# Kernel optimization log

Hardware: AMD Instinct MI355X
Metric: run time of the kernel (lower is better)

The kernel has to match this reference:

```python
import jax, jax.numpy as jnp
import numpy as np

B, C, H, W, S = 32, 512, 32, 32, 4
HW = H * W
OUT = HW // S  # conv1/conv2 out channels = 256
EPS = 1e-5


def setup_inputs() -> dict:
    key = jax.random.key(0)
    ks = jax.random.split(key, 8)
    d = {}
    d["x"] = jax.random.normal(ks[0], (B, C, H, W), jnp.float32)
    # conv1 / bn1 (operate on x_flat with 'channels' = h*w)
    d["w1"] = jax.random.normal(ks[1], (OUT, HW), jnp.float32) * 0.02
    d["b1"] = jnp.zeros((OUT,), jnp.float32)
    d["g1"] = jnp.ones((OUT,), jnp.float32)
    d["be1"] = jnp.zeros((OUT,), jnp.float32)
    d["m1"] = jax.random.normal(ks[2], (OUT,), jnp.float32) * 0.01
    d["v1"] = jnp.ones((OUT,), jnp.float32)
    # conv2 / bn2
    d["w2"] = jax.random.normal(ks[3], (OUT, HW), jnp.float32) * 0.02
    d["b2"] = jnp.zeros((OUT,), jnp.float32)
    d["g2"] = jnp.ones((OUT,), jnp.float32)
    d["be2"] = jnp.zeros((OUT,), jnp.float32)
    d["m2"] = jax.random.normal(ks[4], (OUT,), jnp.float32) * 0.01
    d["v2"] = jnp.ones((OUT,), jnp.float32)
    # conv3 / bn3 (1x1 conv on the real channel dim c)
    d["w3"] = jax.random.normal(ks[5], (C, C), jnp.float32) * 0.02
    d["b3"] = jnp.zeros((C,), jnp.float32)
    d["g3"] = jnp.ones((C,), jnp.float32)
    d["be3"] = jnp.zeros((C,), jnp.float32)
    d["m3"] = jax.random.normal(ks[6], (C,), jnp.float32) * 0.01
    d["v3"] = jnp.ones((C,), jnp.float32)
    # conv4: 1x1 conv mapping 1+2c channels -> 1
    d["w4"] = jax.random.normal(ks[7], (1 + 2 * C,), jnp.float32) * 0.02
    d["b4"] = jnp.zeros((), jnp.float32)
    return d


def _bn1d(t, g, be, m, v):
    # t: [b, o, c]; BatchNorm (eval mode) over channel axis 1
    scale = g / jnp.sqrt(v + EPS)
    return (t - m[:, None]) * scale[:, None] + be[:, None]


def reference(x, w1, b1, g1, be1, m1, v1,
              w2, b2, g2, be2, m2, v2,
              w3, b3, g3, be3, m3, v3,
              w4, b4):
    b, c, h, w = x.shape
    # x_flat: [b, h*w, c] -- conv1/conv2 are 1x1 convs over 'channels' = h*w
    xf = x.reshape(b, c, h * w).transpose(0, 2, 1)
    theta = jax.nn.relu(_bn1d(jnp.einsum('oq,bqc->boc', w1, xf) + b1[:, None],
                              g1, be1, m1, v1))  # [b, OUT, c]
    phi = jax.nn.relu(_bn1d(jnp.einsum('oq,bqc->boc', w2, xf) + b2[:, None],
                            g2, be2, m2, v2))    # [b, OUT, c]
    # per-batch conv2d-as-matmul loop collapses to one batched GEMM:
    # affinity[b, i, j] = sum_k phi[b, k, i] * theta[b, k, j]
    aff = jnp.einsum('bki,bkj->bij', phi, theta)  # [b, c, c]
    # x_embed: 1x1 conv + BN + ReLU + global average pool -> [b, c]
    scale3 = g3 / jnp.sqrt(v3 + EPS)
    xe = jnp.einsum('oc,bchw->bohw', w3, x) + b3[:, None, None]
    xe = jax.nn.relu((xe - m3[:, None, None]) * scale3[:, None, None]
                     + be3[:, None, None])
    xe = xe.mean(axis=(2, 3))  # [b, c]
    # conv4 over y = cat([x_embed, affinity_a, affinity_b], dim=1):
    # affinity_a[b,i,0,p] = aff[b,i,p]; affinity_b[b,i,0,p] = aff[b,p,i]
    logits = (w4[0] * xe
              + jnp.einsum('i,bip->bp', w4[1:1 + c], aff)
              + jnp.einsum('i,bpi->bp', w4[1 + c:], aff)
              + b4)
    a = jax.nn.sigmoid(logits)  # [b, c]
    return x * a[:, :, None, None]
```

## Files before the change

kernel.cpp:

```cpp
#include <hip/hip_runtime.h>
#include <math.h>

#define BB   32
#define CC   512
#define HWW  1024
#define OUTC 256
#define EPSV 1e-5f

typedef __attribute__((ext_vector_type(8))) short bfrag;
typedef __attribute__((ext_vector_type(4))) float f32x4;

__device__ inline unsigned short f2bf(float x){
  unsigned int uu = __float_as_uint(x);
  uu += 0x7fff + ((uu >> 16) & 1);
  return (unsigned short)(uu >> 16);
}
__device__ inline float bf2f(unsigned short h){
  return __uint_as_float(((unsigned int)h) << 16);
}

#define ASYNC16(g, l) \
  __builtin_amdgcn_global_load_lds((const __attribute__((address_space(1))) unsigned int*)(g), \
                                   (__attribute__((address_space(3))) unsigned int*)(l), 16, 0, 0)


__global__ __launch_bounds__(256) void prep(
    const float* __restrict__ x,
    const float* __restrict__ w1, const float* __restrict__ w2,
    const float* __restrict__ w3,
    unsigned short* __restrict__ Xhi, unsigned short* __restrict__ Xlo,
    unsigned short* __restrict__ XThi,
    unsigned short* __restrict__ Whi, unsigned short* __restrict__ Wlo,
    unsigned short* __restrict__ W3hi,
    float* __restrict__ accz)
{
  if (blockIdx.z == 32) {
    int worker = (blockIdx.y * 16 + blockIdx.x) * 256 + threadIdx.x;
    accz[worker] = 0.f;
    for (int i = worker; i < 786432; i += 32768) {
      if (i < 524288) {
        float v = (i < 262144) ? w1[i] : w2[i - 262144];
        unsigned short h = f2bf(v);
        Whi[i] = h;
        Wlo[i] = f2bf(v - bf2f(h));
      } else {
        int j = i - 524288;
        W3hi[j] = f2bf(w3[j]);
      }
    }
    return;
  }
  __shared__ float T[64][65];
  const int b = blockIdx.z, c0 = blockIdx.y * 64, p0 = blockIdx.x * 64;
  const int tid = threadIdx.x, tr = tid >> 4, tc4 = (tid & 15) * 4;
  const float* xb = x + (size_t)b * 512 * 1024;
#pragma unroll
  for (int r = 0; r < 4; ++r) {
    int c = c0 + tr + r * 16;
    float4 v = *(const float4*)(xb + (size_t)c * 1024 + p0 + tc4);
    T[tr + r * 16][tc4 + 0] = v.x; T[tr + r * 16][tc4 + 1] = v.y;
    T[tr + r * 16][tc4 + 2] = v.z; T[tr + r * 16][tc4 + 3] = v.w;
    ushort4 h, l;
    h.x = f2bf(v.x); l.x = f2bf(v.x - bf2f(h.x));
    h.y = f2bf(v.y); l.y = f2bf(v.y - bf2f(h.y));
    h.z = f2bf(v.z); l.z = f2bf(v.z - bf2f(h.z));
    h.w = f2bf(v.w); l.w = f2bf(v.w - bf2f(h.w));
    size_t idx = (size_t)b * 524288 + (size_t)c * 1024 + p0 + tc4;
    *(ushort4*)(Xhi + idx) = h;
    *(ushort4*)(Xlo + idx) = l;
  }
  __syncthreads();
#pragma unroll
  for (int r = 0; r < 4; ++r) {
    int pl = tr + r * 16;
    ushort4 h;
    h.x = f2bf(T[tc4 + 0][pl]); h.y = f2bf(T[tc4 + 1][pl]);
    h.z = f2bf(T[tc4 + 2][pl]); h.w = f2bf(T[tc4 + 3][pl]);
    *(ushort4*)(XThi + (size_t)b * 524288 + (size_t)(p0 + pl) * 512 + c0 + tc4) = h;
  }
}

__global__ __launch_bounds__(256) void gemm_fused(
    const unsigned short* __restrict__ Xhi, const unsigned short* __restrict__ Xlo,
    const unsigned short* __restrict__ Whi, const unsigned short* __restrict__ Wlo,
    const unsigned short* __restrict__ W3hi, const unsigned short* __restrict__ XThi,
    const float* __restrict__ b1p, const float* __restrict__ g1p,
    const float* __restrict__ be1p, const float* __restrict__ m1p, const float* __restrict__ v1p,
    const float* __restrict__ b2p, const float* __restrict__ g2p,
    const float* __restrict__ be2p, const float* __restrict__ m2p, const float* __restrict__ v2p,
    const float* __restrict__ b3p, const float* __restrict__ g3p,
    const float* __restrict__ be3p, const float* __restrict__ m3p, const float* __restrict__ v3p,
    const float* __restrict__ w4,
    float* __restrict__ P2, float* __restrict__ u, float* __restrict__ t,
    float* __restrict__ xe_acc)
{
  __shared__ unsigned short smem[12288];
  const int fid  = blockIdx.x;
  const int tid  = threadIdx.x;
  const int wave = tid >> 6, lane = tid & 63;
  const int lr = lane >> 2;
  const int lcs = ((lane & 3) ^ (lr & 3)) * 8;
  const int fr = lane & 15, fq = lane >> 4;
  const int fsw = (fq ^ (fr & 3)) * 8;

  if (fid < 1024) {
    unsigned short* sAh = smem;
    unsigned short* sAl = smem + 4096;
    unsigned short* sBh = smem + 8192;
    unsigned short* sBl = smem + 10240;
    const int xcd = fid & 7;
    const int n0  = ((fid >> 3) & 7) * 64;
    const int bc  = ((fid >> 6) << 3) | xcd;
    const int b   = bc >> 2;
    const int c0  = (bc & 3) * 128;
    const int wm = wave & 1, wn = wave >> 1;

    const unsigned short* gb; unsigned short* lb; int ninst;
    if (wave == 0)      { gb = Xhi + (size_t)b * 524288 + (size_t)c0 * 1024; lb = sAh; ninst = 8; }
    else if (wave == 1) { gb = Xlo + (size_t)b * 524288 + (size_t)c0 * 1024; lb = sAl; ninst = 8; }
    else if (wave == 2) { gb = Whi + (size_t)n0 * 1024; lb = sBh; ninst = 4; }
    else                { gb = Wlo + (size_t)n0 * 1024; lb = sBl; ninst = 4; }
    gb += (size_t)lr * 1024 + lcs;

    f32x4 acc[4][2];
    const f32x4 zz = {0.f, 0.f, 0.f, 0.f};
#pragma unroll
    for (int i = 0; i < 4; ++i) { acc[i][0] = zz; acc[i][1] = zz; }

    for (int kq = 0; kq < 1024; kq += 32) {
      for (int inst = 0; inst < ninst; ++inst)
        ASYNC16(gb + (size_t)inst * 16 * 1024 + kq, lb + inst * 512);
      __syncthreads();
      bfrag ah[4], al[4], bh[2], bl[2];
#pragma unroll
      for (int i = 0; i < 4; ++i) {
        int off = (wm * 64 + i * 16 + fr) * 32 + fsw;
        ah[i] = *(const bfrag*)&sAh[off];
        al[i] = *(const bfrag*)&sAl[off];
      }
#pragma unroll
      for (int j = 0; j < 2; ++j) {
        int off = (wn * 32 + j * 16 + fr) * 32 + fsw;
        bh[j] = *(const bfrag*)&sBh[off];
        bl[j] = *(const bfrag*)&sBl[off];
      }
#pragma unroll
      for (int i = 0; i < 4; ++i)
#pragma unroll
        for (int j = 0; j < 2; ++j) {
          acc[i][j] = __builtin_amdgcn_mfma_f32_16x16x32_bf16(ah[i], bh[j], acc[i][j], 0, 0, 0);
          acc[i][j] = __builtin_amdgcn_mfma_f32_16x16x32_bf16(ah[i], bl[j], acc[i][j], 0, 0, 0);
          acc[i][j] = __builtin_amdgcn_mfma_f32_16x16x32_bf16(al[i], bh[j], acc[i][j], 0, 0, 0);
        }
      __syncthreads();
    }

    const float *bias, *gg, *bes, *mm, *vv_; int cof;
    if (n0 < 256) { bias = b1p; gg = g1p; bes = be1p; mm = m1p; vv_ = v1p; cof = 0; }
    else          { bias = b2p; gg = g2p; bes = be2p; mm = m2p; vv_ = v2p; cof = 256; }
    const float* wsel = (n0 < 256) ? (w4 + 513) : (w4 + 1);
    float* dsel = (n0 < 256) ? (t + b * 256) : (u + b * 256);
    const int cobase = (n0 - cof) + wn * 32;
    float wt[4][4];
#pragma unroll
    for (int i = 0; i < 4; ++i)
#pragma unroll
      for (int r = 0; r < 4; ++r)
        wt[i][r] = wsel[c0 + wm * 64 + i * 16 + fq * 4 + r];

#pragma unroll
    for (int j = 0; j < 2; ++j) {
      int co = n0 + wn * 32 + j * 16 + fr;
      int q = co - cof;
      float s  = gg[q] * rsqrtf(vv_[q] + EPSV);
      float sh = (bias[q] - mm[q]) * s + bes[q];
      float psum = 0.f;
#pragma unroll
      for (int i = 0; i < 4; ++i) {
        int crow = c0 + wm * 64 + i * 16 + fq * 4;
        float* dst = P2 + ((size_t)b * 512 + crow) * 512 + co;
#pragma unroll
        for (int r = 0; r < 4; ++r) {
          float val = fmaxf(acc[i][j][r] * s + sh, 0.f);
          dst[(size_t)r * 512] = val;
          psum += wt[i][r] * val;
        }
      }
      psum += __shfl_xor(psum, 16);
      psum += __shfl_xor(psum, 32);
      if (fq == 0) atomicAdd(&dsel[cobase + j * 16 + fr], psum);
    }
  } else {
    unsigned short* sA = smem;
    unsigned short* sB = smem + 4096;
    const int h  = fid - 1024;
    const int n0 = (h & 7) * 128;
    const int m0 = ((h >> 3) & 3) * 128;
    const int b  = h >> 5;
    const int wm = wave & 1, wn = wave >> 1;

    const unsigned short* gb; unsigned short* lb;
    if (wave < 2) { gb = W3hi + (size_t)(m0 + wave * 64) * 512; lb = sA + wave * 2048; }
    else { gb = XThi + (size_t)b * 524288 + (size_t)(n0 + (wave - 2) * 64) * 512; lb = sB + (wave - 2) * 2048; }
    gb += (size_t)lr * 512 + lcs;

    f32x4 acc[4][4];
    const f32x4 zz = {0.f, 0.f, 0.f, 0.f};
#pragma unroll
    for (int i = 0; i < 4; ++i)
#pragma unroll
      for (int j = 0; j < 4; ++j) acc[i][j] = zz;

    for (int kq = 0; kq < 512; kq += 32) {
#pragma unroll
      for (int inst = 0; inst < 4; ++inst)
        ASYNC16(gb + (size_t)inst * 16 * 512 + kq, lb + inst * 512);
      __syncthreads();
      bfrag af[4], bf[4];
#pragma unroll
      for (int i = 0; i < 4; ++i)
        af[i] = *(const bfrag*)&sA[(wm * 64 + i * 16 + fr) * 32 + fsw];
#pragma unroll
      for (int j = 0; j < 4; ++j)
        bf[j] = *(const bfrag*)&sB[(wn * 64 + j * 16 + fr) * 32 + fsw];
#pragma unroll
      for (int i = 0; i < 4; ++i)
#pragma unroll
        for (int j = 0; j < 4; ++j)
          acc[i][j] = __builtin_amdgcn_mfma_f32_16x16x32_bf16(af[i], bf[j], acc[i][j], 0, 0, 0);
      __syncthreads();
    }

#pragma unroll
    for (int i = 0; i < 4; ++i) {
#pragma unroll
      for (int r = 0; r < 4; ++r) {
        int o = m0 + wm * 64 + i * 16 + fq * 4 + r;
        float s  = g3p[o] * rsqrtf(v3p[o] + EPSV);
        float sh = (b3p[o] - m3p[o]) * s + be3p[o];
        float v = fmaxf(acc[i][0][r] * s + sh, 0.f) + fmaxf(acc[i][1][r] * s + sh, 0.f)
                + fmaxf(acc[i][2][r] * s + sh, 0.f) + fmaxf(acc[i][3][r] * s + sh, 0.f);
        v += __shfl_xor(v, 1); v += __shfl_xor(v, 2);
        v += __shfl_xor(v, 4); v += __shfl_xor(v, 8);
        if (fr == 0) atomicAdd(&xe_acc[b * 512 + o], v);
      }
    }
  }
}

__global__ __launch_bounds__(256) void k4_gate_out(
    const float* __restrict__ P2, const float* __restrict__ u,
    const float* __restrict__ t, const float* __restrict__ xe_acc,
    const float* __restrict__ w4, const float* __restrict__ b4,
    const float* __restrict__ x, float* __restrict__ out)
{
  __shared__ float us[256], ts[256];
  const int b = blockIdx.x;
  us[threadIdx.x] = u[b * 256 + threadIdx.x];
  ts[threadIdx.x] = t[b * 256 + threadIdx.x];
  __syncthreads();
  const int wave = threadIdx.x >> 6, lane = threadIdx.x & 63;
  const int p = blockIdx.y * 4 + wave;
  const float* row = P2 + ((size_t)b * 512 + p) * 512;
  float4 th = *(const float4*)&row[lane * 4];
  float4 ph = *(const float4*)&row[256 + lane * 4];
  int ki = lane * 4;
  float rs = th.x * us[ki] + th.y * us[ki + 1] + th.z * us[ki + 2] + th.w * us[ki + 3]
           + ph.x * ts[ki] + ph.y * ts[ki + 1] + ph.z * ts[ki + 2] + ph.w * ts[ki + 3];
  rs += __shfl_xor(rs, 1);  rs += __shfl_xor(rs, 2);  rs += __shfl_xor(rs, 4);
  rs += __shfl_xor(rs, 8);  rs += __shfl_xor(rs, 16); rs += __shfl_xor(rs, 32);
  float xe = xe_acc[b * 512 + p] * (1.f / 1024.f);
  float logit = w4[0] * xe + rs + b4[0];
  float a = 1.f / (1.f + expf(-logit));
  const float4* xr = (const float4*)(x + ((size_t)b * 512 + p) * 1024);
  float4* orow = (float4*)(out + ((size_t)b * 512 + p) * 1024);
#pragma unroll
  for (int r2 = 0; r2 < 4; ++r2) {
    float4 xv = xr[lane + r2 * 64];
    float4 ov; ov.x = xv.x * a; ov.y = xv.y * a; ov.z = xv.z * a; ov.w = xv.w * a;
    orow[lane + r2 * 64] = ov;
  }
}

__global__ __launch_bounds__(256) void k1_theta_phi(
    const float* __restrict__ x,
    const float* __restrict__ w1, const float* __restrict__ b1,
    const float* __restrict__ g1, const float* __restrict__ be1,
    const float* __restrict__ m1, const float* __restrict__ v1,
    const float* __restrict__ w2, const float* __restrict__ b2,
    const float* __restrict__ g2, const float* __restrict__ be2,
    const float* __restrict__ m2, const float* __restrict__ v2,
    float* __restrict__ P)
{
  __shared__ __align__(16) float Ws[32][68];
  __shared__ __align__(16) float Xs[32][68];
  const int b  = blockIdx.z;
  const int o0 = blockIdx.y * 64;
  const int c0 = blockIdx.x * 64;
  const int tid = threadIdx.x;
  const int tx = tid & 15, ty = tid >> 4;
  const float* __restrict__ Wbase = (o0 < OUTC) ? (w1 + (size_t)o0 * HWW)
                                                : (w2 + (size_t)(o0 - OUTC) * HWW);
  const float* __restrict__ xb = x + (size_t)b * CC * HWW;
  float acc[4][4] = {{0.f}};
  for (int k0 = 0; k0 < HWW; k0 += 32) {
#pragma unroll
    for (int r = 0; r < 2; ++r) {
      int id  = tid + (r << 8);
      int row = id >> 3;
      int cg  = (id & 7) << 2;
      float4 wv = *(const float4*)(Wbase + (size_t)row * HWW + k0 + cg);
      Ws[cg+0][row] = wv.x; Ws[cg+1][row] = wv.y; Ws[cg+2][row] = wv.z; Ws[cg+3][row] = wv.w;
      float4 xv = *(const float4*)(xb + (size_t)(c0 + row) * HWW + k0 + cg);
      Xs[cg+0][row] = xv.x; Xs[cg+1][row] = xv.y; Xs[cg+2][row] = xv.z; Xs[cg+3][row] = xv.w;
    }
    __syncthreads();
#pragma unroll
    for (int k = 0; k < 32; ++k) {
      float4 av = *(const float4*)&Ws[k][ty * 4];
      float4 bv = *(const float4*)&Xs[k][tx * 4];
      acc[0][0] += av.x*bv.x; acc[0][1] += av.x*bv.y; acc[0][2] += av.x*bv.z; acc[0][3] += av.x*bv.w;
      acc[1][0] += av.y*bv.x; acc[1][1] += av.y*bv.y; acc[1][2] += av.y*bv.z; acc[1][3] += av.y*bv.w;
      acc[2][0] += av.z*bv.x; acc[2][1] += av.z*bv.y; acc[2][2] += av.z*bv.z; acc[2][3] += av.z*bv.w;
      acc[3][0] += av.w*bv.x; acc[3][1] += av.w*bv.y; acc[3][2] += av.w*bv.z; acc[3][3] += av.w*bv.w;
    }
    __syncthreads();
  }
  const float *bias, *g, *be, *m, *v; int ob;
  if (o0 < OUTC) { bias = b1; g = g1; be = be1; m = m1; v = v1; ob = o0; }
  else           { bias = b2; g = g2; be = be2; m = m2; v = v2; ob = o0 - OUTC; }
#pragma unroll
  for (int i = 0; i < 4; ++i) {
    int oi = ob + ty * 4 + i;
    float sc = g[oi] * rsqrtf(v[oi] + EPSV);
    float sh = be[oi] - m[oi] * sc;
    float bb = bias[oi];
    float4 ov;
    ov.x = fmaxf((acc[i][0] + bb) * sc + sh, 0.f);
    ov.y = fmaxf((acc[i][1] + bb) * sc + sh, 0.f);
    ov.z = fmaxf((acc[i][2] + bb) * sc + sh, 0.f);
    ov.w = fmaxf((acc[i][3] + bb) * sc + sh, 0.f);
    int oo = o0 + ty * 4 + i;
    *(float4*)(P + ((size_t)b * 512 + oo) * 512 + c0 + tx * 4) = ov;
  }
}

__global__ __launch_bounds__(256) void k2_xe(
    const float* __restrict__ x, const float* __restrict__ w3,
    const float* __restrict__ b3, const float* __restrict__ g3,
    const float* __restrict__ be3, const float* __restrict__ m3,
    const float* __restrict__ v3, float* __restrict__ xe_acc)
{
  __shared__ __align__(16) float As[32][68];
  __shared__ __align__(16) float Bs[32][68];
  const int b  = blockIdx.z;
  const int o0 = blockIdx.y * 64;
  const int p0 = blockIdx.x * 64;
  const int tid = threadIdx.x;
  const int tx = tid & 15, ty = tid >> 4;
  const float* __restrict__ xb = x + (size_t)b * CC * HWW;
  float acc[4][4] = {{0.f}};
  for (int ck = 0; ck < CC; ck += 32) {
#pragma unroll
    for (int r = 0; r < 2; ++r) {
      int id  = tid + (r << 8);
      int row = id >> 3;
      int cg  = (id & 7) << 2;
      float4 wv = *(const float4*)(w3 + (size_t)(o0 + row) * CC + ck + cg);
      As[cg+0][row] = wv.x; As[cg+1][row] = wv.y; As[cg+2][row] = wv.z; As[cg+3][row] = wv.w;
      int brow = id >> 4;
      int pg   = (id & 15) << 2;
      float4 xv = *(const float4*)(xb + (size_t)(ck + brow) * HWW + p0 + pg);
      *(float4*)&Bs[brow][pg] = xv;
    }
    __syncthreads();
#pragma unroll
    for (int k = 0; k < 32; ++k) {
      float4 av = *(const float4*)&As[k][ty * 4];
      float4 bv = *(const float4*)&Bs[k][tx * 4];
      acc[0][0] += av.x*bv.x; acc[0][1] += av.x*bv.y; acc[0][2] += av.x*bv.z; acc[0][3] += av.x*bv.w;
      acc[1][0] += av.y*bv.x; acc[1][1] += av.y*bv.y; acc[1][2] += av.y*bv.z; acc[1][3] += av.y*bv.w;
      acc[2][0] += av.z*bv.x; acc[2][1] += av.z*bv.y; acc[2][2] += av.z*bv.z; acc[2][3] += av.z*bv.w;
      acc[3][0] += av.w*bv.x; acc[3][1] += av.w*bv.y; acc[3][2] += av.w*bv.z; acc[3][3] += av.w*bv.w;
    }
    __syncthreads();
  }
#pragma unroll
  for (int i = 0; i < 4; ++i) {
    int oo = o0 + ty * 4 + i;
    float sc = g3[oo] * rsqrtf(v3[oo] + EPSV);
    float sh = be3[oo] - m3[oo] * sc;
    float bb = b3[oo];
    float ps = fmaxf((acc[i][0] + bb) * sc + sh, 0.f)
             + fmaxf((acc[i][1] + bb) * sc + sh, 0.f)
             + fmaxf((acc[i][2] + bb) * sc + sh, 0.f)
             + fmaxf((acc[i][3] + bb) * sc + sh, 0.f);
    ps += __shfl_xor(ps, 1);
    ps += __shfl_xor(ps, 2);
    ps += __shfl_xor(ps, 4);
    ps += __shfl_xor(ps, 8);
    if (tx == 0) atomicAdd(&xe_acc[b * CC + oo], ps);
  }
}

__global__ __launch_bounds__(256) void k3_ut(
    const float* __restrict__ P, const float* __restrict__ w4,
    float* __restrict__ u, float* __restrict__ t)
{
  const int b = blockIdx.x;
  const int wv = threadIdx.x >> 6, lane = threadIdx.x & 63;
  const int k = blockIdx.y * 4 + wv;
  const float* __restrict__ w4a = w4 + 1;
  const float* __restrict__ w4b = w4 + 1 + CC;
  const float* __restrict__ throw_ = P + ((size_t)b * 512 + k) * 512;
  const float* __restrict__ phrow  = P + ((size_t)b * 512 + 256 + k) * 512;
  float su = 0.f, st = 0.f;
#pragma unroll
  for (int i = lane; i < CC; i += 64) {
    su += w4a[i] * phrow[i];
    st += w4b[i] * throw_[i];
  }
#pragma unroll
  for (int off = 32; off > 0; off >>= 1) {
    su += __shfl_down(su, off);
    st += __shfl_down(st, off);
  }
  if (lane == 0) { u[b * OUTC + k] = su; t[b * OUTC + k] = st; }
}

__global__ __launch_bounds__(256) void k4_gate(
    const float* __restrict__ P, const float* __restrict__ u,
    const float* __restrict__ t, const float* __restrict__ xe_acc,
    const float* __restrict__ w4, const float* __restrict__ b4,
    float* __restrict__ amul)
{
  __shared__ float us[256], ts[256];
  const int b = blockIdx.x;
  const int p = blockIdx.y * 256 + threadIdx.x;
  us[threadIdx.x] = u[b * OUTC + threadIdx.x];
  ts[threadIdx.x] = t[b * OUTC + threadIdx.x];
  __syncthreads();
  const float* __restrict__ theta = P + (size_t)b * 512 * 512;
  const float* __restrict__ phi   = theta + 256 * 512;
  float r = 0.f, s = 0.f;
#pragma unroll 8
  for (int k = 0; k < OUTC; ++k) {
    r += us[k] * theta[(size_t)k * 512 + p];
    s += ts[k] * phi[(size_t)k * 512 + p];
  }
  float xe = xe_acc[b * CC + p] * (1.0f / 1024.0f);
  float logit = w4[0] * xe + r + s + b4[0];
  amul[b * CC + p] = 1.0f / (1.0f + expf(-logit));
}

__global__ __launch_bounds__(256) void k5_out(
    const float* __restrict__ x, const float* __restrict__ amul,
    float* __restrict__ out)
{
  int i = blockIdx.x * 256 + threadIdx.x;
  float4 xv = ((const float4*)x)[i];
  float a = amul[i >> 8];
  float4 ov; ov.x = xv.x * a; ov.y = xv.y * a; ov.z = xv.z * a; ov.w = xv.w * a;
  ((float4*)out)[i] = ov;
}

extern "C" void kernel_launch(void* const* d_in, const int* in_sizes, int n_in,
                              void* d_out, int out_size, void* d_ws, size_t ws_size,
                              hipStream_t stream)
{
  (void)in_sizes; (void)n_in; (void)out_size;
  const float* x   = (const float*)d_in[0];
  const float* w1  = (const float*)d_in[1];
  const float* b1  = (const float*)d_in[2];
  const float* g1  = (const float*)d_in[3];
  const float* be1 = (const float*)d_in[4];
  const float* m1  = (const float*)d_in[5];
  const float* v1  = (const float*)d_in[6];
  const float* w2  = (const float*)d_in[7];
  const float* b2  = (const float*)d_in[8];
  const float* g2  = (const float*)d_in[9];
  const float* be2 = (const float*)d_in[10];
  const float* m2  = (const float*)d_in[11];
  const float* v2  = (const float*)d_in[12];
  const float* w3  = (const float*)d_in[13];
  const float* b3  = (const float*)d_in[14];
  const float* g3  = (const float*)d_in[15];
  const float* be3 = (const float*)d_in[16];
  const float* m3  = (const float*)d_in[17];
  const float* v3  = (const float*)d_in[18];
  const float* w4  = (const float*)d_in[19];
  const float* b4  = (const float*)d_in[20];
  float* out = (float*)d_out;

  if (ws_size >= 136970240ull) {
    float* P2     = (float*)d_ws;
    float* xe_acc = P2 + 8388608;
    float* u      = P2 + 8404992;
    float* t      = P2 + 8413184;
    unsigned short* Xhi  = (unsigned short*)((char*)d_ws + 33685504);
    unsigned short* Xlo  = Xhi + 16777216;
    unsigned short* XThi = Xlo + 16777216;
    unsigned short* Whi  = XThi + 16777216;
    unsigned short* Wlo  = Whi + 524288;
    unsigned short* W3hi = Wlo + 524288;

    prep<<<dim3(16, 8, 33), 256, 0, stream>>>(x, w1, w2, w3, Xhi, Xlo, XThi,
                                              Whi, Wlo, W3hi, xe_acc);
    gemm_fused<<<dim3(2048), 256, 0, stream>>>(Xhi, Xlo, Whi, Wlo, W3hi, XThi,
        b1, g1, be1, m1, v1, b2, g2, be2, m2, v2, b3, g3, be3, m3, v3,
        w4, P2, u, t, xe_acc);
    k4_gate_out<<<dim3(32, 128), 256, 0, stream>>>(P2, u, t, xe_acc, w4, b4, x, out);
  } else {
    float* P      = (float*)d_ws;
    float* xe_acc = P + (size_t)BB * 512 * 512;
    float* u      = xe_acc + BB * CC;
    float* t      = u + BB * OUTC;
    float* amul   = t + BB * OUTC;

    hipMemsetAsync(xe_acc, 0, (size_t)BB * CC * sizeof(float), stream);

    dim3 blk(256);
    k1_theta_phi<<<dim3(8, 8, BB), blk, 0, stream>>>(x, w1, b1, g1, be1, m1, v1,
                                                     w2, b2, g2, be2, m2, v2, P);
    k2_xe<<<dim3(16, 8, BB), blk, 0, stream>>>(x, w3, b3, g3, be3, m3, v3, xe_acc);
    k3_ut<<<dim3(BB, 64), blk, 0, stream>>>(P, w4, u, t);
    k4_gate<<<dim3(BB, 2), blk, 0, stream>>>(P, u, t, xe_acc, w4, b4, amul);
    k5_out<<<dim3((BB * CC * HWW / 4) / 256), blk, 0, stream>>>(x, amul, out);
  }
}
```

Before: 289.5 us.

## Double-buffer LDS tiles with async prefetch in both fused GEMM paths

```diff
diff --git a/kernel.cpp b/kernel.cpp
--- a/kernel.cpp
+++ b/kernel.cpp
@@ -22,6 +22,8 @@
 #define ASYNC16(g, l) \
   __builtin_amdgcn_global_load_lds((const __attribute__((address_space(1))) unsigned int*)(g), \
                                    (__attribute__((address_space(3))) unsigned int*)(l), 16, 0, 0)
+
+#define WAITV(N) asm volatile("s_waitcnt vmcnt(" #N ")" ::: "memory")
 
 
 __global__ __launch_bounds__(256) void prep(
@@ -94,7 +96,7 @@
     float* __restrict__ P2, float* __restrict__ u, float* __restrict__ t,
     float* __restrict__ xe_acc)
 {
-  __shared__ unsigned short smem[12288];
+  __shared__ unsigned short smem[24576];
   const int fid  = blockIdx.x;
   const int tid  = threadIdx.x;
   const int wave = tid >> 6, lane = tid & 63;
@@ -104,10 +106,6 @@
   const int fsw = (fq ^ (fr & 3)) * 8;
 
   if (fid < 1024) {
-    unsigned short* sAh = smem;
-    unsigned short* sAl = smem + 4096;
-    unsigned short* sBh = smem + 8192;
-    unsigned short* sBl = smem + 10240;
     const int xcd = fid & 7;
     const int n0  = ((fid >> 3) & 7) * 64;
     const int bc  = ((fid >> 6) << 3) | xcd;
@@ -115,11 +113,11 @@
     const int c0  = (bc & 3) * 128;
     const int wm = wave & 1, wn = wave >> 1;
 
-    const unsigned short* gb; unsigned short* lb; int ninst;
-    if (wave == 0)      { gb = Xhi + (size_t)b * 524288 + (size_t)c0 * 1024; lb = sAh; ninst = 8; }
-    else if (wave == 1) { gb = Xlo + (size_t)b * 524288 + (size_t)c0 * 1024; lb = sAl; ninst = 8; }
-    else if (wave == 2) { gb = Whi + (size_t)n0 * 1024; lb = sBh; ninst = 4; }
-    else                { gb = Wlo + (size_t)n0 * 1024; lb = sBl; ninst = 4; }
+    const unsigned short* gb; int lboff; int ninst;
+    if (wave == 0)      { gb = Xhi + (size_t)b * 524288 + (size_t)c0 * 1024; lboff = 0;     ninst = 8; }
+    else if (wave == 1) { gb = Xlo + (size_t)b * 524288 + (size_t)c0 * 1024; lboff = 4096;  ninst = 8; }
+    else if (wave == 2) { gb = Whi + (size_t)n0 * 1024; lboff = 8192;  ninst = 4; }
+    else                { gb = Wlo + (size_t)n0 * 1024; lboff = 10240; ninst = 4; }
     gb += (size_t)lr * 1024 + lcs;
 
     f32x4 acc[4][2];
@@ -127,10 +125,28 @@
 #pragma unroll
     for (int i = 0; i < 4; ++i) { acc[i][0] = zz; acc[i][1] = zz; }
 
+    for (int inst = 0; inst < ninst; ++inst)
+      ASYNC16(gb + (size_t)inst * 16 * 1024, smem + lboff + inst * 512);
+
+    int cur = 0;
     for (int kq = 0; kq < 1024; kq += 32) {
-      for (int inst = 0; inst < ninst; ++inst)
-        ASYNC16(gb + (size_t)inst * 16 * 1024 + kq, lb + inst * 512);
-      __syncthreads();
+      __builtin_amdgcn_sched_barrier(0);
+      if (kq + 32 < 1024) {
+        unsigned short* nb = smem + (cur ^ 1) * 12288 + lboff;
+        for (int inst = 0; inst < ninst; ++inst)
+          ASYNC16(gb + (size_t)inst * 16 * 1024 + kq + 32, nb + inst * 512);
+        if (wave < 2) WAITV(8); else WAITV(4);
+      } else {
+        WAITV(0);
+      }
+      __builtin_amdgcn_s_barrier();
+      __builtin_amdgcn_sched_barrier(0);
+
+      const unsigned short* bufc = smem + cur * 12288;
+      const unsigned short* sAh = bufc;
+      const unsigned short* sAl = bufc + 4096;
+      const unsigned short* sBh = bufc + 8192;
+      const unsigned short* sBl = bufc + 10240;
       bfrag ah[4], al[4], bh[2], bl[2];
 #pragma unroll
       for (int i = 0; i < 4; ++i) {
@@ -152,8 +168,11 @@
           acc[i][j] = __builtin_amdgcn_mfma_f32_16x16x32_bf16(ah[i], bl[j], acc[i][j], 0, 0, 0);
           acc[i][j] = __builtin_amdgcn_mfma_f32_16x16x32_bf16(al[i], bh[j], acc[i][j], 0, 0, 0);
         }
-      __syncthreads();
-    }
+      __builtin_amdgcn_sched_barrier(0);
+      __builtin_amdgcn_s_barrier();
+      cur ^= 1;
+    }
+    __builtin_amdgcn_sched_barrier(0);
 
     const float *bias, *gg, *bes, *mm, *vv_; int cof;
     if (n0 < 256) { bias = b1p; gg = g1p; bes = be1p; mm = m1p; vv_ = v1p; cof = 0; }
@@ -191,17 +210,15 @@
       if (fq == 0) atomicAdd(&dsel[cobase + j * 16 + fr], psum);
     }
   } else {
-    unsigned short* sA = smem;
-    unsigned short* sB = smem + 4096;
     const int h  = fid - 1024;
     const int n0 = (h & 7) * 128;
     const int m0 = ((h >> 3) & 3) * 128;
     const int b  = h >> 5;
     const int wm = wave & 1, wn = wave >> 1;
 
-    const unsigned short* gb; unsigned short* lb;
-    if (wave < 2) { gb = W3hi + (size_t)(m0 + wave * 64) * 512; lb = sA + wave * 2048; }
-    else { gb = XThi + (size_t)b * 524288 + (size_t)(n0 + (wave - 2) * 64) * 512; lb = sB + (wave - 2) * 2048; }
+    const unsigned short* gb; int lboff;
+    if (wave < 2) { gb = W3hi + (size_t)(m0 + wave * 64) * 512; lboff = wave * 2048; }
+    else { gb = XThi + (size_t)b * 524288 + (size_t)(n0 + (wave - 2) * 64) * 512; lboff = 4096 + (wave - 2) * 2048; }
     gb += (size_t)lr * 512 + lcs;
 
     f32x4 acc[4][4];
@@ -211,11 +228,28 @@
 #pragma unroll
       for (int j = 0; j < 4; ++j) acc[i][j] = zz;
 
+#pragma unroll
+    for (int inst = 0; inst < 4; ++inst)
+      ASYNC16(gb + (size_t)inst * 16 * 512, smem + lboff + inst * 512);
+
+    int cur = 0;
     for (int kq = 0; kq < 512; kq += 32) {
-#pragma unroll
-      for (int inst = 0; inst < 4; ++inst)
-        ASYNC16(gb + (size_t)inst * 16 * 512 + kq, lb + inst * 512);
-      __syncthreads();
+      __builtin_amdgcn_sched_barrier(0);
+      if (kq + 32 < 512) {
+        unsigned short* nb = smem + (cur ^ 1) * 8192 + lboff;
+#pragma unroll
+        for (int inst = 0; inst < 4; ++inst)
+          ASYNC16(gb + (size_t)inst * 16 * 512 + kq + 32, nb + inst * 512);
+        WAITV(4);
+      } else {
+        WAITV(0);
+      }
+      __builtin_amdgcn_s_barrier();
+      __builtin_amdgcn_sched_barrier(0);
+
+      const unsigned short* bufc = smem + cur * 8192;
+      const unsigned short* sA = bufc;
+      const unsigned short* sB = bufc + 4096;
       bfrag af[4], bf[4];
 #pragma unroll
       for (int i = 0; i < 4; ++i)
@@ -228,8 +262,11 @@
 #pragma unroll
         for (int j = 0; j < 4; ++j)
           acc[i][j] = __builtin_amdgcn_mfma_f32_16x16x32_bf16(af[i], bf[j], acc[i][j], 0, 0, 0);
-      __syncthreads();
-    }
+      __builtin_amdgcn_sched_barrier(0);
+      __builtin_amdgcn_s_barrier();
+      cur ^= 1;
+    }
+    __builtin_amdgcn_sched_barrier(0);
 
 #pragma unroll
     for (int i = 0; i < 4; ++i) {
```

Result: no change. 287.1 us (-0.8%).

## Pre-swizzle operands into MFMA fragment layout and load directly from global

Applied to the files above, without the earlier changes.

```diff
diff --git a/kernel.cpp b/kernel.cpp
--- a/kernel.cpp
+++ b/kernel.cpp
@@ -18,10 +18,6 @@
 __device__ inline float bf2f(unsigned short h){
   return __uint_as_float(((unsigned int)h) << 16);
 }
-
-#define ASYNC16(g, l) \
-  __builtin_amdgcn_global_load_lds((const __attribute__((address_space(1))) unsigned int*)(g), \
-                                   (__attribute__((address_space(3))) unsigned int*)(l), 16, 0, 0)
 
 
 __global__ __launch_bounds__(256) void prep(
@@ -41,11 +37,17 @@
       if (i < 524288) {
         float v = (i < 262144) ? w1[i] : w2[i - 262144];
         unsigned short h = f2bf(v);
-        Whi[i] = h;
-        Wlo[i] = f2bf(v - bf2f(h));
+        int o = i >> 10, k = i & 1023;
+        int fw = (((o >> 4) * 32 + (k >> 5)) * 512)
+               + ((k >> 3) & 3) * 128 + (o & 15) * 8 + (k & 7);
+        Whi[fw] = h;
+        Wlo[fw] = f2bf(v - bf2f(h));
       } else {
         int j = i - 524288;
-        W3hi[j] = f2bf(w3[j]);
+        int o = j >> 9, c = j & 511;
+        int fw = (((o >> 4) * 16 + (c >> 5)) * 512)
+               + ((c >> 3) & 3) * 128 + (o & 15) * 8 + (c & 7);
+        W3hi[fw] = f2bf(w3[j]);
       }
     }
     return;
@@ -57,7 +59,8 @@
 #pragma unroll
   for (int r = 0; r < 4; ++r) {
     int c = c0 + tr + r * 16;
-    float4 v = *(const float4*)(xb + (size_t)c * 1024 + p0 + tc4);
+    int p = p0 + tc4;
+    float4 v = *(const float4*)(xb + (size_t)c * 1024 + p);
     T[tr + r * 16][tc4 + 0] = v.x; T[tr + r * 16][tc4 + 1] = v.y;
     T[tr + r * 16][tc4 + 2] = v.z; T[tr + r * 16][tc4 + 3] = v.w;
     ushort4 h, l;
@@ -65,22 +68,28 @@
     h.y = f2bf(v.y); l.y = f2bf(v.y - bf2f(h.y));
     h.z = f2bf(v.z); l.z = f2bf(v.z - bf2f(h.z));
     h.w = f2bf(v.w); l.w = f2bf(v.w - bf2f(h.w));
-    size_t idx = (size_t)b * 524288 + (size_t)c * 1024 + p0 + tc4;
+    size_t idx = (size_t)b * 524288
+               + ((size_t)(c >> 4) * 32 + (p >> 5)) * 512
+               + ((p >> 3) & 3) * 128 + (c & 15) * 8 + (p & 7);
     *(ushort4*)(Xhi + idx) = h;
     *(ushort4*)(Xlo + idx) = l;
   }
   __syncthreads();
 #pragma unroll
   for (int r = 0; r < 4; ++r) {
-    int pl = tr + r * 16;
+    int pl = p0 + tr + r * 16;
+    int cc = c0 + tc4;
     ushort4 h;
-    h.x = f2bf(T[tc4 + 0][pl]); h.y = f2bf(T[tc4 + 1][pl]);
-    h.z = f2bf(T[tc4 + 2][pl]); h.w = f2bf(T[tc4 + 3][pl]);
-    *(ushort4*)(XThi + (size_t)b * 524288 + (size_t)(p0 + pl) * 512 + c0 + tc4) = h;
-  }
-}
-
-__global__ __launch_bounds__(256) void gemm_fused(
+    h.x = f2bf(T[tc4 + 0][tr + r * 16]); h.y = f2bf(T[tc4 + 1][tr + r * 16]);
+    h.z = f2bf(T[tc4 + 2][tr + r * 16]); h.w = f2bf(T[tc4 + 3][tr + r * 16]);
+    size_t idx = (size_t)b * 524288
+               + ((size_t)(pl >> 4) * 16 + (cc >> 5)) * 512
+               + ((cc >> 3) & 3) * 128 + (pl & 15) * 8 + (cc & 7);
+    *(ushort4*)(XThi + idx) = h;
+  }
+}
+
+__global__ __launch_bounds__(256, 3) void gemm_fused(
     const unsigned short* __restrict__ Xhi, const unsigned short* __restrict__ Xlo,
     const unsigned short* __restrict__ Whi, const unsigned short* __restrict__ Wlo,
     const unsigned short* __restrict__ W3hi, const unsigned short* __restrict__ XThi,
@@ -94,20 +103,12 @@
     float* __restrict__ P2, float* __restrict__ u, float* __restrict__ t,
     float* __restrict__ xe_acc)
 {
-  __shared__ unsigned short smem[12288];
   const int fid  = blockIdx.x;
   const int tid  = threadIdx.x;
   const int wave = tid >> 6, lane = tid & 63;
-  const int lr = lane >> 2;
-  const int lcs = ((lane & 3) ^ (lr & 3)) * 8;
   const int fr = lane & 15, fq = lane >> 4;
-  const int fsw = (fq ^ (fr & 3)) * 8;
 
   if (fid < 1024) {
-    unsigned short* sAh = smem;
-    unsigned short* sAl = smem + 4096;
-    unsigned short* sBh = smem + 8192;
-    unsigned short* sBl = smem + 10240;
     const int xcd = fid & 7;
     const int n0  = ((fid >> 3) & 7) * 64;
     const int bc  = ((fid >> 6) << 3) | xcd;
@@ -115,34 +116,30 @@
     const int c0  = (bc & 3) * 128;
     const int wm = wave & 1, wn = wave >> 1;
 
-    const unsigned short* gb; unsigned short* lb; int ninst;
-    if (wave == 0)      { gb = Xhi + (size_t)b * 524288 + (size_t)c0 * 1024; lb = sAh; ninst = 8; }
-    else if (wave == 1) { gb = Xlo + (size_t)b * 524288 + (size_t)c0 * 1024; lb = sAl; ninst = 8; }
-    else if (wave == 2) { gb = Whi + (size_t)n0 * 1024; lb = sBh; ninst = 4; }
-    else                { gb = Wlo + (size_t)n0 * 1024; lb = sBl; ninst = 4; }
-    gb += (size_t)lr * 1024 + lcs;
+    const bfrag* Ah = (const bfrag*)Xhi + (size_t)b * 65536
+                    + (size_t)((c0 >> 4) + wm * 4) * 2048 + lane;
+    const bfrag* Al = (const bfrag*)Xlo + (size_t)b * 65536
+                    + (size_t)((c0 >> 4) + wm * 4) * 2048 + lane;
+    const bfrag* Bh = (const bfrag*)Whi + (size_t)((n0 >> 4) + wn * 2) * 2048 + lane;
+    const bfrag* Bl = (const bfrag*)Wlo + (size_t)((n0 >> 4) + wn * 2) * 2048 + lane;
 
     f32x4 acc[4][2];
     const f32x4 zz = {0.f, 0.f, 0.f, 0.f};
 #pragma unroll
     for (int i = 0; i < 4; ++i) { acc[i][0] = zz; acc[i][1] = zz; }
 
-    for (int kq = 0; kq < 1024; kq += 32) {
-      for (int inst = 0; inst < ninst; ++inst)
-        ASYNC16(gb + (size_t)inst * 16 * 1024 + kq, lb + inst * 512);
-      __syncthreads();
-      bfrag ah[4], al[4], bh[2], bl[2];
+#pragma unroll 2
+    for (int kq = 0; kq < 32; ++kq) {
+      bfrag bh[2], bl[2], ah[4], al[4];
+#pragma unroll
+      for (int j = 0; j < 2; ++j) {
+        bh[j] = Bh[(size_t)j * 2048 + kq * 64];
+        bl[j] = Bl[(size_t)j * 2048 + kq * 64];
+      }
 #pragma unroll
       for (int i = 0; i < 4; ++i) {
-        int off = (wm * 64 + i * 16 + fr) * 32 + fsw;
-        ah[i] = *(const bfrag*)&sAh[off];
-        al[i] = *(const bfrag*)&sAl[off];
-      }
-#pragma unroll
-      for (int j = 0; j < 2; ++j) {
-        int off = (wn * 32 + j * 16 + fr) * 32 + fsw;
-        bh[j] = *(const bfrag*)&sBh[off];
-        bl[j] = *(const bfrag*)&sBl[off];
+        ah[i] = Ah[(size_t)i * 2048 + kq * 64];
+        al[i] = Al[(size_t)i * 2048 + kq * 64];
       }
 #pragma unroll
       for (int i = 0; i < 4; ++i)
@@ -152,7 +149,6 @@
           acc[i][j] = __builtin_amdgcn_mfma_f32_16x16x32_bf16(ah[i], bl[j], acc[i][j], 0, 0, 0);
           acc[i][j] = __builtin_amdgcn_mfma_f32_16x16x32_bf16(al[i], bh[j], acc[i][j], 0, 0, 0);
         }
-      __syncthreads();
     }
 
     const float *bias, *gg, *bes, *mm, *vv_; int cof;
@@ -191,18 +187,15 @@
       if (fq == 0) atomicAdd(&dsel[cobase + j * 16 + fr], psum);
     }
   } else {
-    unsigned short* sA = smem;
-    unsigned short* sB = smem + 4096;
     const int h  = fid - 1024;
     const int n0 = (h & 7) * 128;
     const int m0 = ((h >> 3) & 3) * 128;
     const int b  = h >> 5;
     const int wm = wave & 1, wn = wave >> 1;
 
-    const unsigned short* gb; unsigned short* lb;
-    if (wave < 2) { gb = W3hi + (size_t)(m0 + wave * 64) * 512; lb = sA + wave * 2048; }
-    else { gb = XThi + (size_t)b * 524288 + (size_t)(n0 + (wave - 2) * 64) * 512; lb = sB + (wave - 2) * 2048; }
-    gb += (size_t)lr * 512 + lcs;
+    const bfrag* Af = (const bfrag*)W3hi + (size_t)((m0 >> 4) + wm * 4) * 1024 + lane;
+    const bfrag* Bf = (const bfrag*)XThi + (size_t)b * 65536
+                    + (size_t)((n0 >> 4) + wn * 4) * 1024 + lane;
 
     f32x4 acc[4][4];
     const f32x4 zz = {0.f, 0.f, 0.f, 0.f};
@@ -211,24 +204,20 @@
 #pragma unroll
       for (int j = 0; j < 4; ++j) acc[i][j] = zz;
 
-    for (int kq = 0; kq < 512; kq += 32) {
-#pragma unroll
-      for (int inst = 0; inst < 4; ++inst)
-        ASYNC16(gb + (size_t)inst * 16 * 512 + kq, lb + inst * 512);
-      __syncthreads();
-      bfrag af[4], bf[4];
+#pragma unroll 2
+    for (int kq = 0; kq < 16; ++kq) {
+      bfrag af[4], bf4[4];
 #pragma unroll
       for (int i = 0; i < 4; ++i)
-        af[i] = *(const bfrag*)&sA[(wm * 64 + i * 16 + fr) * 32 + fsw];
+        af[i] = Af[(size_t)i * 1024 + kq * 64];
 #pragma unroll
       for (int j = 0; j < 4; ++j)
-        bf[j] = *(const bfrag*)&sB[(wn * 64 + j * 16 + fr) * 32 + fsw];
+        bf4[j] = Bf[(size_t)j * 1024 + kq * 64];
 #pragma unroll
       for (int i = 0; i < 4; ++i)
 #pragma unroll
         for (int j = 0; j < 4; ++j)
-          acc[i][j] = __builtin_amdgcn_mfma_f32_16x16x32_bf16(af[i], bf[j], acc[i][j], 0, 0, 0);
-      __syncthreads();
+          acc[i][j] = __builtin_amdgcn_mfma_f32_16x16x32_bf16(af[i], bf4[j], acc[i][j], 0, 0, 0);
     }
 
 #pragma unroll
```

Result: no change. 284.3 us (-1.8%).
